# Optimization experiments

Hardware: AMD Instinct MI355X
Metric: run time of the kernel (lower is better)

## Reference

```python
import jax, jax.numpy as jnp
import numpy as np

LAYERS = 2
HIDDEN = 512
FFN = 2048
HEADS = 8
IMG = (32, 64)
SLEN = IMG[0] * IMG[1]
BSZ = 2
KEY_DIM = HIDDEN // HEADS      # 64
V_DIM = HIDDEN * 2             # 1024
HEAD_SIZE = V_DIM // HEADS     # 128
SCALE_BASE = 512.0
SCALING = KEY_DIM ** (-0.5)
LN_EPS = 1e-5


def xpos_apply(x):
    # x: [..., L, d]  (XPOS rotary with length-dependent decay, downscale=False)
    L, d = x.shape[-2], x.shape[-1]
    half = d // 2
    base = (jnp.arange(0, d, 2, dtype=jnp.float32) + 0.4 * d) / (1.4 * d)  # [half]
    min_pos = -(L // 2)
    pos = jnp.arange(min_pos, L + min_pos, dtype=jnp.float32)              # [L]
    scale = base[None, :] ** (pos[:, None] / SCALE_BASE)                   # [L, half]
    inv_freq = 1.0 / (10000.0 ** (jnp.arange(half, dtype=jnp.float32) / half))
    sinusoid = jnp.arange(L, dtype=jnp.float32)[:, None] * inv_freq[None, :]  # [L, half]
    sin = jnp.repeat(jnp.sin(sinusoid) * scale, 2, axis=-1)                # [L, d]
    cos = jnp.repeat(jnp.cos(sinusoid) * scale, 2, axis=-1)                # [L, d]
    x1 = x[..., 0::2]
    x2 = x[..., 1::2]
    rot = jnp.stack([-x2, x1], axis=-1).reshape(x.shape)  # rotate_every_two
    return x * cos + rot * sin


def layer_norm(x, g, b):
    mu = jnp.mean(x, axis=-1, keepdims=True)
    var = jnp.mean(jnp.square(x - mu), axis=-1, keepdims=True)
    return (x - mu) * jax.lax.rsqrt(var + LN_EPS) * g + b


def attention(x, Wq, Wk, Wv, Wo):
    B, S, _ = x.shape
    q = (x @ Wq).reshape(B, S, HEADS, KEY_DIM).transpose(0, 2, 1, 3)   # [B,H,S,dk]
    k = (x @ Wk).reshape(B, S, HEADS, KEY_DIM).transpose(0, 2, 1, 3)
    v = (x @ Wv).reshape(B, S, HEADS, HEAD_SIZE).transpose(0, 2, 1, 3)  # [B,H,S,hs]
    q = xpos_apply(q)
    k = xpos_apply(k)
    scores = jnp.einsum('bhqd,bhkd->bhqk', q, k)
    att = jax.nn.softmax(scores.astype(jnp.float32), axis=-1).astype(scores.dtype)
    att = att * SCALING  # note: scaling applied AFTER softmax, as in the source
    out = jnp.einsum('bhqk,bhkv->bhqv', att, v)                          # [B,H,S,hs]
    out = out.transpose(0, 2, 1, 3).reshape(B, S, V_DIM)
    return out @ Wo


def setup_inputs() -> dict:
    key = jax.random.key(0)
    ks = jax.random.split(key, 8)
    p = lambda k, shp: jax.random.normal(k, shp, dtype=jnp.float32) * 0.02
    return {
        'x':  jax.random.normal(ks[0], (BSZ, SLEN, HIDDEN), dtype=jnp.float32),
        'Wq': p(ks[1], (LAYERS, HIDDEN, HIDDEN)),
        'Wk': p(ks[2], (LAYERS, HIDDEN, HIDDEN)),
        'Wv': p(ks[3], (LAYERS, HIDDEN, V_DIM)),
        'Wo': p(ks[4], (LAYERS, V_DIM, HIDDEN)),
        'W1': p(ks[5], (LAYERS, HIDDEN, FFN)),
        'b1': jnp.zeros((LAYERS, FFN), jnp.float32),
        'W2': p(ks[6], (LAYERS, FFN, HIDDEN)),
        'b2': jnp.zeros((LAYERS, HIDDEN), jnp.float32),
        'g1': jnp.ones((LAYERS, HIDDEN), jnp.float32),
        'be1': jnp.zeros((LAYERS, HIDDEN), jnp.float32),
        'g2': jnp.ones((LAYERS, HIDDEN), jnp.float32),
        'be2': jnp.zeros((LAYERS, HIDDEN), jnp.float32),
    }


def reference(x, Wq, Wk, Wv, Wo, W1, b1, W2, b2, g1, be1, g2, be2):
    for i in range(LAYERS):
        y = layer_norm(x + attention(x, Wq[i], Wk[i], Wv[i], Wo[i]), g1[i], be1[i])
        ffn = jax.nn.relu(y @ W1[i] + b1[i]) @ W2[i] + b2[i]
        x = layer_norm(y + ffn, g2[i], be2[i])
    return x.reshape(x.shape[0], IMG[0], IMG[1], x.shape[2])
```

## Files before the change

kernel.cpp:

```cpp
#include <hip/hip_runtime.h>
#include <hip/hip_bf16.h>
#include <math.h>

#define LAYERS 2
#define HIDDEN 512
#define FFN_DIM 2048
#define HEADS 8
#define SLEN 2048
#define BSZ 2
#define MROWS 4096
#define ATT_SCALING 0.125f
#define LN_EPS 1e-5f
#define SCALE_BASE 512.0f
#define LOG2E 1.4426950408889634f

typedef unsigned short u16;
typedef unsigned int u32;
typedef __attribute__((ext_vector_type(8))) short bf16x8;
typedef __attribute__((ext_vector_type(4))) float f32x4;

__device__ __forceinline__ float bf2f(u16 u) {
    union { u32 i; float f; } v; v.i = ((u32)u) << 16; return v.f;
}
__device__ __forceinline__ u16 f2bf(float f) {
    union { float f; u32 i; } v; v.f = f;
    u32 r = v.i + 0x7FFFu + ((v.i >> 16) & 1u);
    return (u16)(r >> 16);
}
__device__ __forceinline__ u32 pk2bf(float a, float b) {
    union { __hip_bfloat162 h; u32 u; } v;
    v.h = __float22bfloat162_rn(make_float2(a, b));
    return v.u;
}
__device__ __forceinline__ void async16(const void* g, void* l) {
    __builtin_amdgcn_global_load_lds((const __attribute__((address_space(1))) void*)g,
                                     (__attribute__((address_space(3))) void*)l, 16, 0, 0);
}

__global__ __launch_bounds__(256) void prep_kernel(const float* __restrict__ x,
                                                   const float* __restrict__ Wq,
                                                   const float* __restrict__ Wk,
                                                   const float* __restrict__ Wv,
                                                   const float* __restrict__ Wo,
                                                   const float* __restrict__ W1,
                                                   const float* __restrict__ W2,
                                                   char* __restrict__ w,
                                                   float* __restrict__ Af,
                                                   u16* __restrict__ Ab,
                                                   float2* __restrict__ tab) {
    const size_t MB1 = 1u << 20;
    const int bid = blockIdx.x;
    const int tid = threadIdx.x;
    __shared__ float t[32][33];

    if (bid < 7168) {
        int l = bid / 3584;
        int tt = bid % 3584;
        u16* WqkvT = (u16*)(w + 48 * MB1 + (size_t)l * 2 * MB1);
        u16* WoT   = (u16*)(w + 52 * MB1 + (size_t)l * 1 * MB1);
        u16* W1T   = (u16*)(w + 54 * MB1 + (size_t)l * 2 * MB1);
        u16* W2T   = (u16*)(w + 58 * MB1 + (size_t)l * 2 * MB1);
        const float* src; u16* dst; int K, N, tix;
        if (tt < 256)       { src = Wq + (size_t)l * 512 * 512;  dst = WqkvT;              K = 512;  N = 512;  tix = tt; }
        else if (tt < 512)  { src = Wk + (size_t)l * 512 * 512;  dst = WqkvT + 512 * 512;  K = 512;  N = 512;  tix = tt - 256; }
        else if (tt < 1024) { src = Wv + (size_t)l * 512 * 1024; dst = WqkvT + 1024 * 512; K = 512;  N = 1024; tix = tt - 512; }
        else if (tt < 1536) { src = Wo + (size_t)l * 1024 * 512; dst = WoT;                K = 1024; N = 512;  tix = tt - 1024; }
        else if (tt < 2560) { src = W1 + (size_t)l * 512 * 2048; dst = W1T;                K = 512;  N = 2048; tix = tt - 1536; }
        else                { src = W2 + (size_t)l * 2048 * 512; dst = W2T;                K = 2048; N = 512;  tix = tt - 2560; }
        int ntx = N >> 5;
        int n0 = (tix % ntx) * 32, k0 = (tix / ntx) * 32;
        int tx = tid & 31, ty = tid >> 5;
#pragma unroll
        for (int i = 0; i < 4; i++)
            t[ty + 8 * i][tx] = src[(size_t)(k0 + ty + 8 * i) * N + n0 + tx];
        __syncthreads();
#pragma unroll
        for (int i = 0; i < 4; i++)
            dst[(size_t)(n0 + ty + 8 * i) * K + k0 + tx] = f2bf(t[tx][ty + 8 * i]);
    } else if (bid < 9216) {
        int i = ((bid - 7168) * 256 + tid) * 4;
        float4 v = *(const float4*)(x + i);
        *(float4*)(Af + i) = v;
        uint2 p;
        p.x = pk2bf(v.x, v.y);
        p.y = pk2bf(v.z, v.w);
        *(uint2*)(Ab + i) = p;
    } else {
        int idx = (bid - 9216) * 256 + tid;
        int j = idx & 31;
        int s = idx >> 5;
        float base = (2.0f * j + 0.4f * 64.0f) / (1.4f * 64.0f);
        float pos = (float)(s - 1024);
        float scale = powf(base, pos / SCALE_BASE);
        float inv_freq = powf(10000.0f, -(float)j / 32.0f);
        float ang = (float)s * inv_freq;
        tab[idx] = make_float2(cosf(ang) * scale, sinf(ang) * scale);
    }
}

__global__ __launch_bounds__(256) void xpos_vtrans(u16* __restrict__ QKV,
                                                   const float2* __restrict__ tab,
                                                   u16* __restrict__ VT) {
    const int bid = blockIdx.x;
    const int tid = threadIdx.x;
    __shared__ u16 t[64][65];

    if (bid < 4096) {
        int idx = bid * 256 + tid;
        int j = idx & 31;
        int h = (idx >> 5) & 7;
        int s = (idx >> 8) & 2047;
        int b = idx >> 19;

        float2 cssn = tab[s * 32 + j];
        float cs = cssn.x, sn = cssn.y;

        size_t off = (size_t)(b * SLEN + s) * 2048 + h * 64 + 2 * j;
        u32* pq = (u32*)(QKV + off);
        u32* pk = (u32*)(QKV + off + 512);

        u32 qv = *pq;
        float q0 = bf2f((u16)(qv & 0xffff)), q1 = bf2f((u16)(qv >> 16));
        *pq = pk2bf((q0 * cs - q1 * sn) * LOG2E, (q1 * cs + q0 * sn) * LOG2E);

        u32 kv = *pk;
        float k0 = bf2f((u16)(kv & 0xffff)), k1 = bf2f((u16)(kv >> 16));
        *pk = pk2bf(k0 * cs - k1 * sn, k1 * cs + k0 * sn);
    } else {
        int v = bid - 4096;
        int bz = v & 15;
        int vy = (v >> 4) & 1;
        int sx = v >> 5;
        int b = bz >> 3, h = bz & 7;
        int s0 = sx * 64, v0 = vy * 64;
#pragma unroll
        for (int i = 0; i < 16; i++) {
            int e = tid + i * 256; int r = e >> 6, c = e & 63;
            t[r][c] = QKV[(size_t)(b * SLEN + s0 + r) * 2048 + 1024 + h * 128 + v0 + c];
        }
        __syncthreads();
#pragma unroll
        for (int i = 0; i < 16; i++) {
            int e = tid + i * 256; int r = e >> 6, c = e & 63;
            VT[(size_t)((b * 8 + h) * 128 + v0 + r) * 2048 + s0 + c] = t[c][r];
        }
    }
}

template <int BM, int BN, int BK, int WM, int OUTF32, int BIAS, int RELU, int NSPLIT>
__global__ __launch_bounds__(256) void gemm_mfma(const u16* __restrict__ A,
                                                 const u16* __restrict__ WT,
                                                 const float* __restrict__ bias,
                                                 void* __restrict__ C0,
                                                 void* __restrict__ C1,
                                                 int M, int N, int K) {
    constexpr int WN  = 4 / WM;
    constexpr int AM  = BM / (WM * 16);
    constexpr int AN  = BN / (WN * 16);
    constexpr int KO  = BK / 32;
    constexpr int AIT = BM * BK / 2048;
    constexpr int BIT = BN * BK / 2048;
    constexpr int KB8 = BK / 8;

    __shared__ u16 As[2][BM * BK];
    __shared__ u16 Bs[2][BN * BK];

    const int tid  = threadIdx.x;
    const int wave = tid >> 6;
    const int lane = tid & 63;
    const int quad = lane >> 4;
    const int l15  = lane & 15;
    const int wm = wave % WM;
    const int wn = wave / WM;

    const int tm = blockIdx.y * BM;
    const int tn = blockIdx.x * BN;
    const int z  = (NSPLIT > 1) ? blockIdx.z : 0;
    const int Ksub = K / NSPLIT;
    const int k0g  = z * Ksub;

    auto issue = [&](int kt, int buf) {
#pragma unroll
        for (int it = 0; it < AIT; it++) {
            int cid = it * 256 + tid;
            async16(A + (size_t)(tm + cid / KB8) * K + k0g + kt + (cid % KB8) * 8,
                    (char*)As[buf] + (it * 256 + wave * 64) * 16);
        }
#pragma unroll
        for (int it = 0; it < BIT; it++) {
            int cid = it * 256 + tid;
            async16(WT + (size_t)(tn + cid / KB8) * K + k0g + kt + (cid % KB8) * 8,
                    (char*)Bs[buf] + (it * 256 + wave * 64) * 16);
        }
    };

    f32x4 acc[AM][AN];
#pragma unroll
    for (int i = 0; i < AM; i++)
#pragma unroll
        for (int j = 0; j < AN; j++) acc[i][j] = (f32x4){0.f, 0.f, 0.f, 0.f};

    const int nk = Ksub / BK;
    issue(0, 0);

    for (int t = 0; t < nk; t++) {
        __syncthreads();
        if (t + 1 < nk) issue((t + 1) * BK, (t + 1) & 1);
        const int buf = t & 1;

        bf16x8 af[KO][AM], bfr[KO][AN];
#pragma unroll
        for (int ko = 0; ko < KO; ko++) {
#pragma unroll
            for (int i = 0; i < AM; i++)
                af[ko][i] = *(const bf16x8*)((const char*)As[buf] +
                    (((wm * (AM * 16) + i * 16 + l15) * KB8) + ko * 4 + quad) * 16);
#pragma unroll
            for (int j = 0; j < AN; j++)
                bfr[ko][j] = *(const bf16x8*)((const char*)Bs[buf] +
                    (((wn * (AN * 16) + j * 16 + l15) * KB8) + ko * 4 + quad) * 16);
        }
#pragma unroll
        for (int ko = 0; ko < KO; ko++)
#pragma unroll
            for (int i = 0; i < AM; i++)
#pragma unroll
                for (int j = 0; j < AN; j++)
                    acc[i][j] = __builtin_amdgcn_mfma_f32_16x16x32_bf16(
                        af[ko][i], bfr[ko][j], acc[i][j], 0, 0, 0);
    }

    void* Cout = (NSPLIT > 1 && z) ? C1 : C0;
#pragma unroll
    for (int i = 0; i < AM; i++) {
#pragma unroll
        for (int j = 0; j < AN; j++) {
            int col = tn + wn * (AN * 16) + j * 16 + l15;
            float bv = (BIAS && z == 0) ? bias[col] : 0.0f;
#pragma unroll
            for (int r = 0; r < 4; r++) {
                int row = tm + wm * (AM * 16) + i * 16 + quad * 4 + r;
                float v = acc[i][j][r] + bv;
                if (RELU) v = fmaxf(v, 0.0f);
                if (OUTF32) ((float*)Cout)[(size_t)row * N + col] = v;
                else        ((u16*)Cout)[(size_t)row * N + col] = f2bf(v);
            }
        }
    }
}

__global__ __launch_bounds__(256, 2) void flash_attn_mfma(const u16* __restrict__ QKV,
                                                          const u16* __restrict__ VT,
                                                          u16* __restrict__ OP0,
                                                          u16* __restrict__ OP1,
                                                          float2* __restrict__ ML) {
    const int h  = blockIdx.x;
    const int q0 = blockIdx.y * 128;
    const int bz = blockIdx.z;
    const int b  = bz >> 1;
    const int split = bz & 1;
    const int tid  = threadIdx.x;
    const int wave = tid >> 6;
    const int lane = tid & 63;
    const int quad = lane >> 4;
    const int l15  = lane & 15;

    __shared__ u16 Ks[2][64 * 64];
    __shared__ u16 Vs[2][128 * 64];

    auto issueKV = [&](int kt, int buf) {
#pragma unroll
        for (int it = 0; it < 2; it++) {
            int cid = it * 256 + tid;
            int c = cid >> 8, p = cid & 255;
            async16(QKV + (size_t)(b * SLEN + kt + (p >> 2)) * 2048 + 512 + h * 64 +
                        c * 32 + (p & 3) * 8,
                    (char*)Ks[buf] + (it * 256 + wave * 64) * 16);
        }
#pragma unroll
        for (int it = 0; it < 4; it++) {
            int cid = it * 256 + tid;
            int c = cid >> 9, p = cid & 511;
            async16(VT + (size_t)((b * 8 + h) * 128 + (p >> 2)) * 2048 + kt +
                        c * 32 + (p & 3) * 8,
                    (char*)Vs[buf] + (it * 256 + wave * 64) * 16);
        }
    };

    bf16x8 qf[2][2];
#pragma unroll
    for (int cn = 0; cn < 2; cn++) {
        const u16* p = QKV + (size_t)(b * SLEN + q0 + cn * 64 + wave * 16 + l15) * 2048 +
                       h * 64 + quad * 8;
        qf[cn][0] = *(const bf16x8*)p;
        qf[cn][1] = *(const bf16x8*)(p + 32);
    }

    f32x4 o_acc[2][8];
#pragma unroll
    for (int cn = 0; cn < 2; cn++)
#pragma unroll
        for (int t = 0; t < 8; t++) o_acc[cn][t] = (f32x4){0.f, 0.f, 0.f, 0.f};
    float m[2] = {-1e30f, -1e30f};
    float l[2] = {0.f, 0.f};

    const int kb0 = split * 1024;
    issueKV(kb0, 0);

    for (int ti = 0; ti < 16; ti++) {
        __syncthreads();
        if (ti + 1 < 16) issueKV(kb0 + (ti + 1) * 64, (ti + 1) & 1);
        const int buf = ti & 1;

        f32x4 st[2][4];
#pragma unroll
        for (int cn = 0; cn < 2; cn++)
#pragma unroll
            for (int t = 0; t < 4; t++) st[cn][t] = (f32x4){0.f, 0.f, 0.f, 0.f};
#pragma unroll
        for (int c = 0; c < 2; c++)
#pragma unroll
            for (int t = 0; t < 4; t++) {
                bf16x8 kb = *(const bf16x8*)((const char*)Ks[buf] + c * 4096 +
                             ((t * 16 + l15) * 4 + quad) * 16);
                st[0][t] = __builtin_amdgcn_mfma_f32_16x16x32_bf16(kb, qf[0][c],
                                                                   st[0][t], 0, 0, 0);
                st[1][t] = __builtin_amdgcn_mfma_f32_16x16x32_bf16(kb, qf[1][c],
                                                                   st[1][t], 0, 0, 0);
            }

        float mx[2], tp[2];
#pragma unroll
        for (int cn = 0; cn < 2; cn++) {
            float v = -1e30f;
#pragma unroll
            for (int t = 0; t < 4; t++)
#pragma unroll
                for (int r = 0; r < 4; r++) v = fmaxf(v, st[cn][t][r]);
            mx[cn] = v;
        }
        tp[0] = __shfl_xor(mx[0], 16, 64); tp[1] = __shfl_xor(mx[1], 16, 64);
        mx[0] = fmaxf(mx[0], tp[0]);       mx[1] = fmaxf(mx[1], tp[1]);
        tp[0] = __shfl_xor(mx[0], 32, 64); tp[1] = __shfl_xor(mx[1], 32, 64);
        mx[0] = fmaxf(mx[0], tp[0]);       mx[1] = fmaxf(mx[1], tp[1]);

        float alpha[2], ls[2];
        u32 pp[2][4][2];
#pragma unroll
        for (int cn = 0; cn < 2; cn++) {
            float mnew = fmaxf(m[cn], mx[cn]);
            alpha[cn] = exp2f(m[cn] - mnew);
            float s = 0.f;
#pragma unroll
            for (int t = 0; t < 4; t++)
#pragma unroll
                for (int pr = 0; pr < 2; pr++) {
                    float p0 = exp2f(st[cn][t][2 * pr] - mnew);
                    float p1 = exp2f(st[cn][t][2 * pr + 1] - mnew);
                    s += p0 + p1;
                    pp[cn][t][pr] = pk2bf(p0, p1);
                }
            ls[cn] = s;
            m[cn] = mnew;
        }
        tp[0] = __shfl_xor(ls[0], 16, 64); tp[1] = __shfl_xor(ls[1], 16, 64);
        ls[0] += tp[0];                    ls[1] += tp[1];
        tp[0] = __shfl_xor(ls[0], 32, 64); tp[1] = __shfl_xor(ls[1], 32, 64);
        ls[0] += tp[0];                    ls[1] += tp[1];
        l[0] = l[0] * alpha[0] + ls[0];
        l[1] = l[1] * alpha[1] + ls[1];

#pragma unroll
        for (int cn = 0; cn < 2; cn++)
#pragma unroll
            for (int t = 0; t < 8; t++)
#pragma unroll
                for (int r = 0; r < 4; r++) o_acc[cn][t][r] *= alpha[cn];

#pragma unroll
        for (int c = 0; c < 2; c++) {
            union { u32 u[4]; bf16x8 v; } pu[2];
#pragma unroll
            for (int j2 = 0; j2 < 4; j2++) {
                int src = (2 * (quad & 1) + (j2 >> 1)) * 16 + l15;
                u32 g0a = (u32)__shfl((int)pp[0][2 * c][j2 & 1], src, 64);
                u32 g1a = (u32)__shfl((int)pp[0][2 * c + 1][j2 & 1], src, 64);
                u32 g0b = (u32)__shfl((int)pp[1][2 * c][j2 & 1], src, 64);
                u32 g1b = (u32)__shfl((int)pp[1][2 * c + 1][j2 & 1], src, 64);
                pu[0].u[j2] = (quad & 2) ? g1a : g0a;
                pu[1].u[j2] = (quad & 2) ? g1b : g0b;
            }
#pragma unroll
            for (int t = 0; t < 8; t++) {
                bf16x8 vb = *(const bf16x8*)((const char*)Vs[buf] + c * 8192 +
                             ((t * 16 + l15) * 4 + quad) * 16);
                o_acc[0][t] = __builtin_amdgcn_mfma_f32_16x16x32_bf16(vb, pu[0].v,
                                                                      o_acc[0][t], 0, 0, 0);
                o_acc[1][t] = __builtin_amdgcn_mfma_f32_16x16x32_bf16(vb, pu[1].v,
                                                                      o_acc[1][t], 0, 0, 0);
            }
        }
    }

    u16* OP = split ? OP1 : OP0;
#pragma unroll
    for (int cn = 0; cn < 2; cn++) {
        if (quad == 0)
            ML[((size_t)(split * 2 + b) * 8 + h) * 2048 + q0 + cn * 64 + wave * 16 + l15] =
                make_float2(m[cn], l[cn]);
        size_t rowbase = ((size_t)(b * SLEN + q0 + cn * 64 + wave * 16 + l15)) * 1024 +
                         h * 128;
#pragma unroll
        for (int t = 0; t < 8; t++)
#pragma unroll
            for (int rp = 0; rp < 2; rp++)
                *(u32*)(OP + rowbase + t * 16 + quad * 4 + 2 * rp) =
                    pk2bf(o_acc[cn][t][2 * rp], o_acc[cn][t][2 * rp + 1]);
    }
}

__global__ __launch_bounds__(256) void attn_combine(const u16* __restrict__ P0,
                                                    const u16* __restrict__ P1,
                                                    const float2* __restrict__ ML,
                                                    u16* __restrict__ AT) {
    int idx = (blockIdx.x * 256 + threadIdx.x) * 8;
    int hv = idx & 1023;
    int row = idx >> 10;
    int h = hv >> 7;
    int b = row >> 11, q = row & 2047;
    float2 ml0 = ML[((size_t)(0 + b) * 8 + h) * 2048 + q];
    float2 ml1 = ML[((size_t)(2 + b) * 8 + h) * 2048 + q];
    float M = fmaxf(ml0.x, ml1.x);
    float w0 = exp2f(ml0.x - M), w1 = exp2f(ml1.x - M);
    float L = ml0.y * w0 + ml1.y * w1;
    float sc = ATT_SCALING / L;
    w0 *= sc; w1 *= sc;

    uint4 a = *(const uint4*)(P0 + idx);
    uint4 c = *(const uint4*)(P1 + idx);
    uint4 o;
    u32 au[4] = {a.x, a.y, a.z, a.w};
    u32 cu[4] = {c.x, c.y, c.z, c.w};
    u32 ou[4];
#pragma unroll
    for (int k = 0; k < 4; k++) {
        float r0 = bf2f((u16)(au[k] & 0xffff)) * w0 + bf2f((u16)(cu[k] & 0xffff)) * w1;
        float r1 = bf2f((u16)(au[k] >> 16)) * w0 + bf2f((u16)(cu[k] >> 16)) * w1;
        ou[k] = pk2bf(r0, r1);
    }
    o.x = ou[0]; o.y = ou[1]; o.z = ou[2]; o.w = ou[3];
    *(uint4*)(AT + idx) = o;
}

__global__ __launch_bounds__(256) void addln_kernel(const float* __restrict__ X,
                                                    const float* __restrict__ R0,
                                                    const float* __restrict__ R1,
                                                    const float* __restrict__ g,
                                                    const float* __restrict__ be,
                                                    float* __restrict__ dstf,
                                                    u16* __restrict__ dstb) {
    const int row = blockIdx.x;
    const int tid = threadIdx.x;
    __shared__ float red[256];
    size_t off = (size_t)row * HIDDEN + 2 * tid;
    float2 a  = *(const float2*)(X + off);
    float2 r0 = *(const float2*)(R0 + off);
    float2 r1 = *(const float2*)(R1 + off);
    float v0 = a.x + r0.x + r1.x;
    float v1 = a.y + r0.y + r1.y;
    red[tid] = v0 + v1;
    __syncthreads();
    for (int s = 128; s > 0; s >>= 1) { if (tid < s) red[tid] += red[tid + s]; __syncthreads(); }
    float mu = red[0] * (1.0f / HIDDEN);
    __syncthreads();
    float d0 = v0 - mu, d1 = v1 - mu;
    red[tid] = d0 * d0 + d1 * d1;
    __syncthreads();
    for (int s = 128; s > 0; s >>= 1) { if (tid < s) red[tid] += red[tid + s]; __syncthreads(); }
    float rstd = rsqrtf(red[0] * (1.0f / HIDDEN) + LN_EPS);
    float2 gg = *(const float2*)(g + 2 * tid);
    float2 bb = *(const float2*)(be + 2 * tid);
    float o0 = d0 * rstd * gg.x + bb.x;
    float o1 = d1 * rstd * gg.y + bb.y;
    *(float2*)(dstf + off) = make_float2(o0, o1);
    *(u32*)(dstb + off) = pk2bf(o0, o1);
}

extern "C" void kernel_launch(void* const* d_in, const int* in_sizes, int n_in,
                              void* d_out, int out_size, void* d_ws, size_t ws_size,
                              hipStream_t stream) {
    const float* x   = (const float*)d_in[0];
    const float* Wq  = (const float*)d_in[1];
    const float* Wk  = (const float*)d_in[2];
    const float* Wv  = (const float*)d_in[3];
    const float* Wo  = (const float*)d_in[4];
    const float* W1  = (const float*)d_in[5];
    const float* b1  = (const float*)d_in[6];
    const float* W2  = (const float*)d_in[7];
    const float* b2  = (const float*)d_in[8];
    const float* g1  = (const float*)d_in[9];
    const float* be1 = (const float*)d_in[10];
    const float* g2  = (const float*)d_in[11];
    const float* be2 = (const float*)d_in[12];
    float* out = (float*)d_out;

    const size_t MB = 1u << 20;
    char* w = (char*)d_ws;
    float*  R1f  = (float*)(w);
    float*  F2a  = (float*)(w);
    u16*    VTg  = (u16*)(w + 8 * MB);
    float*  Yf   = (float*)(w + 8 * MB);
    u16*    OP1  = (u16*)(w + 16 * MB);
    float*  PfA  = (float*)(w + 16 * MB);
    float*  F2b  = (float*)(w + 16 * MB);
    u16*    QKV  = (u16*)(w + 24 * MB);
    float*  PfB  = (float*)(w + 24 * MB);
    u16*    F1   = (u16*)(w + 24 * MB);
    u16*    A_bf = (u16*)(w + 40 * MB);
    u16*    OP0  = (u16*)(w + 40 * MB);
    u16*    AT   = (u16*)(w + 40 * MB);
    u16*    Y_bf = (u16*)(w + 40 * MB);
    float2* xtab = (float2*)(w + 62 * MB);
    float2* ML   = (float2*)(w + 62 * MB + 512 * 1024);

    prep_kernel<<<9472, 256, 0, stream>>>(x, Wq, Wk, Wv, Wo, W1, W2,
                                          w, R1f, A_bf, xtab);

    for (int l = 0; l < LAYERS; l++) {
        u16* WqkvT = (u16*)(w + 48 * MB + (size_t)l * 2 * MB);
        u16* WoT   = (u16*)(w + 52 * MB + (size_t)l * 1 * MB);
        u16* W1T   = (u16*)(w + 54 * MB + (size_t)l * 2 * MB);
        u16* W2T   = (u16*)(w + 58 * MB + (size_t)l * 2 * MB);
        const float* b1_l  = b1 + (size_t)l * FFN_DIM;
        const float* b2_l  = b2 + (size_t)l * HIDDEN;
        const float* g1_l  = g1 + (size_t)l * HIDDEN;
        const float* be1_l = be1 + (size_t)l * HIDDEN;
        const float* g2_l  = g2 + (size_t)l * HIDDEN;
        const float* be2_l = be2 + (size_t)l * HIDDEN;

        gemm_mfma<128, 128, 64, 2, 0, 0, 0, 1><<<dim3(16, 32), 256, 0, stream>>>(
            A_bf, WqkvT, nullptr, QKV, nullptr, MROWS, 2048, 512);

        xpos_vtrans<<<5120, 256, 0, stream>>>(QKV, xtab, VTg);

        flash_attn_mfma<<<dim3(8, 16, 4), 256, 0, stream>>>(QKV, VTg, OP0, OP1, ML);
        attn_combine<<<MROWS * 1024 / 2048, 256, 0, stream>>>(OP0, OP1, ML, AT);

        gemm_mfma<128, 64, 64, 2, 1, 0, 0, 2><<<dim3(8, 32, 2), 256, 0, stream>>>(
            AT, WoT, nullptr, PfA, PfB, MROWS, 512, 1024);

        addln_kernel<<<MROWS, 256, 0, stream>>>(R1f, PfA, PfB, g1_l, be1_l, Yf, Y_bf);

        gemm_mfma<128, 128, 64, 2, 0, 1, 1, 1><<<dim3(16, 32), 256, 0, stream>>>(
            Y_bf, W1T, b1_l, F1, nullptr, MROWS, 2048, 512);

        gemm_mfma<128, 64, 64, 2, 1, 1, 0, 2><<<dim3(8, 32, 2), 256, 0, stream>>>(
            F1, W2T, b2_l, F2a, F2b, MROWS, 512, 2048);

        float* dstf = (l == LAYERS - 1) ? out : R1f;
        addln_kernel<<<MROWS, 256, 0, stream>>>(Yf, F2a, F2b, g2_l, be2_l, dstf, A_bf);
    }
}
```

Measured before the change: 424.8 us.

## Halve flash-attention query tile, swizzle K/V LDS layout, add MFMA priority hints

The flash-attention kernel now processes 64 query rows per block instead of 128, doubling the grid to 1024 blocks and raising launch bounds to 3 blocks per CU so more work is resident. The K and V shared-memory tiles use an XOR swizzle on the 16-byte chunk index to reduce LDS bank conflicts on fragment reads, and MFMA sections are wrapped in s_setprio hints. The trade-off is that each K/V tile loaded into LDS is reused by half as many query rows, so K/V global traffic doubles.

New measurement: 432.4 us. About the same (+1.8%).

```diff
diff --git a/kernel.cpp b/kernel.cpp
--- a/kernel.cpp
+++ b/kernel.cpp
@@ -249,13 +249,13 @@
     }
 }
 
-__global__ __launch_bounds__(256, 2) void flash_attn_mfma(const u16* __restrict__ QKV,
+__global__ __launch_bounds__(256, 3) void flash_attn_mfma(const u16* __restrict__ QKV,
                                                           const u16* __restrict__ VT,
                                                           u16* __restrict__ OP0,
                                                           u16* __restrict__ OP1,
                                                           float2* __restrict__ ML) {
     const int h  = blockIdx.x;
-    const int q0 = blockIdx.y * 128;
+    const int q0 = blockIdx.y * 64;
     const int bz = blockIdx.z;
     const int b  = bz >> 1;
     const int split = bz & 1;
@@ -264,6 +264,7 @@
     const int lane = tid & 63;
     const int quad = lane >> 4;
     const int l15  = lane & 15;
+    const int swz  = quad ^ ((l15 >> 1) & 3);
 
     __shared__ u16 Ks[2][64 * 64];
     __shared__ u16 Vs[2][128 * 64];
@@ -274,7 +275,7 @@
             int cid = it * 256 + tid;
             int c = cid >> 8, p = cid & 255;
             async16(QKV + (size_t)(b * SLEN + kt + (p >> 2)) * 2048 + 512 + h * 64 +
-                        c * 32 + (p & 3) * 8,
+                        c * 32 + (((p & 3) ^ ((p >> 3) & 3)) * 8),
                     (char*)Ks[buf] + (it * 256 + wave * 64) * 16);
         }
 #pragma unroll
@@ -282,27 +283,24 @@
             int cid = it * 256 + tid;
             int c = cid >> 9, p = cid & 511;
             async16(VT + (size_t)((b * 8 + h) * 128 + (p >> 2)) * 2048 + kt +
-                        c * 32 + (p & 3) * 8,
+                        c * 32 + (((p & 3) ^ ((p >> 3) & 3)) * 8),
                     (char*)Vs[buf] + (it * 256 + wave * 64) * 16);
         }
     };
 
-    bf16x8 qf[2][2];
-#pragma unroll
-    for (int cn = 0; cn < 2; cn++) {
-        const u16* p = QKV + (size_t)(b * SLEN + q0 + cn * 64 + wave * 16 + l15) * 2048 +
+    bf16x8 qf[2];
+    {
+        const u16* p = QKV + (size_t)(b * SLEN + q0 + wave * 16 + l15) * 2048 +
                        h * 64 + quad * 8;
-        qf[cn][0] = *(const bf16x8*)p;
-        qf[cn][1] = *(const bf16x8*)(p + 32);
-    }
-
-    f32x4 o_acc[2][8];
-#pragma unroll
-    for (int cn = 0; cn < 2; cn++)
-#pragma unroll
-        for (int t = 0; t < 8; t++) o_acc[cn][t] = (f32x4){0.f, 0.f, 0.f, 0.f};
-    float m[2] = {-1e30f, -1e30f};
-    float l[2] = {0.f, 0.f};
+        qf[0] = *(const bf16x8*)p;
+        qf[1] = *(const bf16x8*)(p + 32);
+    }
+
+    f32x4 o_acc[8];
+#pragma unroll
+    for (int t = 0; t < 8; t++) o_acc[t] = (f32x4){0.f, 0.f, 0.f, 0.f};
+    float m = -1e30f;
+    float l = 0.f;
 
     const int kb0 = split * 1024;
     issueKV(kb0, 0);
@@ -312,111 +310,85 @@
         if (ti + 1 < 16) issueKV(kb0 + (ti + 1) * 64, (ti + 1) & 1);
         const int buf = ti & 1;
 
-        f32x4 st[2][4];
-#pragma unroll
-        for (int cn = 0; cn < 2; cn++)
-#pragma unroll
-            for (int t = 0; t < 4; t++) st[cn][t] = (f32x4){0.f, 0.f, 0.f, 0.f};
+        f32x4 st[4];
+#pragma unroll
+        for (int t = 0; t < 4; t++) st[t] = (f32x4){0.f, 0.f, 0.f, 0.f};
+        __builtin_amdgcn_s_setprio(1);
 #pragma unroll
         for (int c = 0; c < 2; c++)
 #pragma unroll
             for (int t = 0; t < 4; t++) {
                 bf16x8 kb = *(const bf16x8*)((const char*)Ks[buf] + c * 4096 +
-                             ((t * 16 + l15) * 4 + quad) * 16);
-                st[0][t] = __builtin_amdgcn_mfma_f32_16x16x32_bf16(kb, qf[0][c],
-                                                                   st[0][t], 0, 0, 0);
-                st[1][t] = __builtin_amdgcn_mfma_f32_16x16x32_bf16(kb, qf[1][c],
-                                                                   st[1][t], 0, 0, 0);
+                             ((t * 16 + l15) * 4 + swz) * 16);
+                st[t] = __builtin_amdgcn_mfma_f32_16x16x32_bf16(kb, qf[c],
+                                                                st[t], 0, 0, 0);
             }
-
-        float mx[2], tp[2];
-#pragma unroll
-        for (int cn = 0; cn < 2; cn++) {
-            float v = -1e30f;
-#pragma unroll
-            for (int t = 0; t < 4; t++)
-#pragma unroll
-                for (int r = 0; r < 4; r++) v = fmaxf(v, st[cn][t][r]);
-            mx[cn] = v;
-        }
-        tp[0] = __shfl_xor(mx[0], 16, 64); tp[1] = __shfl_xor(mx[1], 16, 64);
-        mx[0] = fmaxf(mx[0], tp[0]);       mx[1] = fmaxf(mx[1], tp[1]);
-        tp[0] = __shfl_xor(mx[0], 32, 64); tp[1] = __shfl_xor(mx[1], 32, 64);
-        mx[0] = fmaxf(mx[0], tp[0]);       mx[1] = fmaxf(mx[1], tp[1]);
-
-        float alpha[2], ls[2];
-        u32 pp[2][4][2];
-#pragma unroll
-        for (int cn = 0; cn < 2; cn++) {
-            float mnew = fmaxf(m[cn], mx[cn]);
-            alpha[cn] = exp2f(m[cn] - mnew);
-            float s = 0.f;
-#pragma unroll
-            for (int t = 0; t < 4; t++)
-#pragma unroll
-                for (int pr = 0; pr < 2; pr++) {
-                    float p0 = exp2f(st[cn][t][2 * pr] - mnew);
-                    float p1 = exp2f(st[cn][t][2 * pr + 1] - mnew);
-                    s += p0 + p1;
-                    pp[cn][t][pr] = pk2bf(p0, p1);
-                }
-            ls[cn] = s;
-            m[cn] = mnew;
-        }
-        tp[0] = __shfl_xor(ls[0], 16, 64); tp[1] = __shfl_xor(ls[1], 16, 64);
-        ls[0] += tp[0];                    ls[1] += tp[1];
-        tp[0] = __shfl_xor(ls[0], 32, 64); tp[1] = __shfl_xor(ls[1], 32, 64);
-        ls[0] += tp[0];                    ls[1] += tp[1];
-        l[0] = l[0] * alpha[0] + ls[0];
-        l[1] = l[1] * alpha[1] + ls[1];
-
-#pragma unroll
-        for (int cn = 0; cn < 2; cn++)
-#pragma unroll
-            for (int t = 0; t < 8; t++)
-#pragma unroll
-                for (int r = 0; r < 4; r++) o_acc[cn][t][r] *= alpha[cn];
+        __builtin_amdgcn_s_setprio(0);
+
+        float mx = -1e30f;
+#pragma unroll
+        for (int t = 0; t < 4; t++)
+#pragma unroll
+            for (int r = 0; r < 4; r++) mx = fmaxf(mx, st[t][r]);
+        mx = fmaxf(mx, __shfl_xor(mx, 16, 64));
+        mx = fmaxf(mx, __shfl_xor(mx, 32, 64));
+
+        float mnew = fmaxf(m, mx);
+        float alpha = exp2f(m - mnew);
+        float s = 0.f;
+        u32 pp[4][2];
+#pragma unroll
+        for (int t = 0; t < 4; t++)
+#pragma unroll
+            for (int pr = 0; pr < 2; pr++) {
+                float p0 = exp2f(st[t][2 * pr] - mnew);
+                float p1 = exp2f(st[t][2 * pr + 1] - mnew);
+                s += p0 + p1;
+                pp[t][pr] = pk2bf(p0, p1);
+            }
+        m = mnew;
+        s += __shfl_xor(s, 16, 64);
+        s += __shfl_xor(s, 32, 64);
+        l = l * alpha + s;
+
+#pragma unroll
+        for (int t = 0; t < 8; t++)
+#pragma unroll
+            for (int r = 0; r < 4; r++) o_acc[t][r] *= alpha;
 
 #pragma unroll
         for (int c = 0; c < 2; c++) {
-            union { u32 u[4]; bf16x8 v; } pu[2];
+            union { u32 u[4]; bf16x8 v; } pu;
 #pragma unroll
             for (int j2 = 0; j2 < 4; j2++) {
                 int src = (2 * (quad & 1) + (j2 >> 1)) * 16 + l15;
-                u32 g0a = (u32)__shfl((int)pp[0][2 * c][j2 & 1], src, 64);
-                u32 g1a = (u32)__shfl((int)pp[0][2 * c + 1][j2 & 1], src, 64);
-                u32 g0b = (u32)__shfl((int)pp[1][2 * c][j2 & 1], src, 64);
-                u32 g1b = (u32)__shfl((int)pp[1][2 * c + 1][j2 & 1], src, 64);
-                pu[0].u[j2] = (quad & 2) ? g1a : g0a;
-                pu[1].u[j2] = (quad & 2) ? g1b : g0b;
+                u32 g0 = (u32)__shfl((int)pp[2 * c][j2 & 1], src, 64);
+                u32 g1 = (u32)__shfl((int)pp[2 * c + 1][j2 & 1], src, 64);
+                pu.u[j2] = (quad & 2) ? g1 : g0;
             }
+            __builtin_amdgcn_s_setprio(1);
 #pragma unroll
             for (int t = 0; t < 8; t++) {
                 bf16x8 vb = *(const bf16x8*)((const char*)Vs[buf] + c * 8192 +
-                             ((t * 16 + l15) * 4 + quad) * 16);
-                o_acc[0][t] = __builtin_amdgcn_mfma_f32_16x16x32_bf16(vb, pu[0].v,
-                                                                      o_acc[0][t], 0, 0, 0);
-                o_acc[1][t] = __builtin_amdgcn_mfma_f32_16x16x32_bf16(vb, pu[1].v,
-                                                                      o_acc[1][t], 0, 0, 0);
+                             ((t * 16 + l15) * 4 + swz) * 16);
+                o_acc[t] = __builtin_amdgcn_mfma_f32_16x16x32_bf16(vb, pu.v,
+                                                                   o_acc[t], 0, 0, 0);
             }
+            __builtin_amdgcn_s_setprio(0);
         }
     }
 
     u16* OP = split ? OP1 : OP0;
-#pragma unroll
-    for (int cn = 0; cn < 2; cn++) {
-        if (quad == 0)
-            ML[((size_t)(split * 2 + b) * 8 + h) * 2048 + q0 + cn * 64 + wave * 16 + l15] =
-                make_float2(m[cn], l[cn]);
-        size_t rowbase = ((size_t)(b * SLEN + q0 + cn * 64 + wave * 16 + l15)) * 1024 +
-                         h * 128;
-#pragma unroll
-        for (int t = 0; t < 8; t++)
-#pragma unroll
-            for (int rp = 0; rp < 2; rp++)
-                *(u32*)(OP + rowbase + t * 16 + quad * 4 + 2 * rp) =
-                    pk2bf(o_acc[cn][t][2 * rp], o_acc[cn][t][2 * rp + 1]);
-    }
+    if (quad == 0)
+        ML[((size_t)(split * 2 + b) * 8 + h) * 2048 + q0 + wave * 16 + l15] =
+            make_float2(m, l);
+    size_t rowbase = ((size_t)(b * SLEN + q0 + wave * 16 + l15)) * 1024 + h * 128;
+#pragma unroll
+    for (int t = 0; t < 8; t++)
+#pragma unroll
+        for (int rp = 0; rp < 2; rp++)
+            *(u32*)(OP + rowbase + t * 16 + quad * 4 + 2 * rp) =
+                pk2bf(o_acc[t][2 * rp], o_acc[t][2 * rp + 1]);
 }
 
 __global__ __launch_bounds__(256) void attn_combine(const u16* __restrict__ P0,
@@ -543,7 +515,7 @@
 
         xpos_vtrans<<<5120, 256, 0, stream>>>(QKV, xtab, VTg);
 
-        flash_attn_mfma<<<dim3(8, 16, 4), 256, 0, stream>>>(QKV, VTg, OP0, OP1, ML);
+        flash_attn_mfma<<<dim3(8, 32, 4), 256, 0, stream>>>(QKV, VTg, OP0, OP1, ML);
         attn_combine<<<MROWS * 1024 / 2048, 256, 0, stream>>>(OP0, OP1, ML, AT);
 
         gemm_mfma<128, 64, 64, 2, 1, 0, 0, 2><<<dim3(8, 32, 2), 256, 0, stream>>>(
```
